# Performance work log

Hardware: AMD Instinct MI355X
Metric: run time of the kernel (lower is better)

Reference implementation:

```python
import jax, jax.numpy as jnp
import numpy as np

N, E, ND, ED, H, OUT, L, VC = 10000, 160000, 8, 4, 128, 256, 6, 6
HEADS, C = 4, 128  # GATConv: out_channels=128 per head, concat=False -> mean over heads


def _ln(x, g, b, eps=1e-5):
    m = x.mean(-1, keepdims=True)
    v = ((x - m) ** 2).mean(-1, keepdims=True)
    return (x - m) * jax.lax.rsqrt(v + eps) * g + b


def _gat_layer(h, src, dst, e_attr, lw, a_src, a_dst, lew, a_edge, bias):
    # h: [N,H]; e_attr: [Etot,H]; PyG GATConv(heads=4, concat=False, edge_dim=H)
    xh = (h @ lw).reshape(N, HEADS, C)                 # [N,4,128]
    eh = (e_attr @ lew).reshape(-1, HEADS, C)          # [Etot,4,128]
    al_s = jnp.einsum('nhc,hc->nh', xh, a_src)
    al_d = jnp.einsum('nhc,hc->nh', xh, a_dst)
    al_e = jnp.einsum('ehc,hc->eh', eh, a_edge)
    alpha = jax.nn.leaky_relu(al_s[src] + al_d[dst] + al_e, 0.2)  # [Etot,4]
    amax = jax.ops.segment_max(alpha, dst, num_segments=N)
    ex = jnp.exp(alpha - amax[dst])
    den = jax.ops.segment_sum(ex, dst, num_segments=N)
    w = ex / (den[dst] + 1e-16)
    out = jax.ops.segment_sum(xh[src] * w[..., None], dst, num_segments=N)  # [N,4,128]
    return out.mean(axis=1) + bias


def setup_inputs() -> dict:
    key = jax.random.key(0)
    ks = jax.random.split(key, 32)
    s = 0.05
    d = {
        'x': jax.random.normal(ks[0], (N, ND), jnp.float32),
        'edge_index': jax.random.randint(ks[1], (2, E), 0, N),
        'edge_attr': jax.random.uniform(ks[2], (E, ED), jnp.float32),
        'vnf_context': jax.random.normal(ks[3], (1, VC), jnp.float32),
        # node embedding
        'node_w': jax.random.normal(ks[4], (ND, H)) * s, 'node_b': jnp.zeros((H,)),
        # EdgeAttentionLayer
        'ea_proj_w': jax.random.normal(ks[5], (ED, H)) * s, 'ea_proj_b': jnp.zeros((H,)),
        'vnf_w': jax.random.normal(ks[6], (VC, H)) * s, 'vnf_b': jnp.zeros((H,)),
        'att1_w': jax.random.normal(ks[7], (2 * H, H)) * s, 'att1_b': jnp.zeros((H,)),
        'att2_w': jax.random.normal(ks[8], (H, H // 2)) * s, 'att2_b': jnp.zeros((H // 2,)),
        'att3_w': jax.random.normal(ks[9], (H // 2, 1)) * s, 'att3_b': jnp.zeros((1,)),
        # per-layer GATConv params (stacked over L layers)
        'gat_lin_w': jax.random.normal(ks[10], (L, H, HEADS * C)) * s,
        'gat_att_src': jax.random.normal(ks[11], (L, HEADS, C)) * s,
        'gat_att_dst': jax.random.normal(ks[12], (L, HEADS, C)) * s,
        'gat_lin_edge_w': jax.random.normal(ks[13], (L, H, HEADS * C)) * s,
        'gat_att_edge': jax.random.normal(ks[14], (L, HEADS, C)) * s,
        'gat_bias': jnp.zeros((L, C)),
        'ln_scale': jnp.ones((L, H)), 'ln_bias': jnp.zeros((L, H)),
        # output projection
        'out_w': jax.random.normal(ks[15], (H, OUT)) * s, 'out_b': jnp.zeros((OUT,)),
    }
    return d


def reference(x, edge_index, edge_attr, vnf_context, node_w, node_b, ea_proj_w, ea_proj_b,
              vnf_w, vnf_b, att1_w, att1_b, att2_w, att2_b, att3_w, att3_b,
              gat_lin_w, gat_att_src, gat_att_dst, gat_lin_edge_w, gat_att_edge, gat_bias,
              ln_scale, ln_bias, out_w, out_b):
    src, dst = edge_index[0], edge_index[1]
    h = x @ node_w + node_b                                   # [N,128]
    # EdgeAttentionLayer (eval mode, no network_state)
    ef = edge_attr @ ea_proj_w + ea_proj_b                    # [E,128]
    vnf = vnf_context @ vnf_w + vnf_b                         # [1,128]
    comb = jnp.concatenate([ef, jnp.broadcast_to(vnf, (E, H))], axis=-1)
    a = jax.nn.relu(comb @ att1_w + att1_b)
    a = jax.nn.relu(a @ att2_w + att2_b)
    e_gate = jax.nn.sigmoid(a @ att3_w + att3_b)              # [E,1]
    w_edge = ef * e_gate                                      # [E,128]
    # GATConv default add_self_loops=True, fill_value='mean'
    loop = jnp.arange(N)
    src2 = jnp.concatenate([src, loop])
    dst2 = jnp.concatenate([dst, loop])
    e2 = jnp.concatenate([w_edge, jnp.broadcast_to(w_edge.mean(0, keepdims=True), (N, H))], axis=0)
    for l in range(L):
        hc = _gat_layer(h, src2, dst2, e2, gat_lin_w[l], gat_att_src[l], gat_att_dst[l],
                        gat_lin_edge_w[l], gat_att_edge[l], gat_bias[l])
        h = _ln(h + jax.nn.relu(hc), ln_scale[l], ln_bias[l])
    return h @ out_w + out_b                                  # [N,256]
```

## Files before the change

### kernel.cpp

```cpp
#include <hip/hip_runtime.h>
#include <hip/hip_bf16.h>
#include <math.h>

#define Nn 10000
#define Ee 160000
#define ET 170000
#define LL 6

typedef short v8s __attribute__((ext_vector_type(8)));
typedef float v4f __attribute__((ext_vector_type(4)));
typedef float v2f __attribute__((ext_vector_type(2)));

__device__ __forceinline__ unsigned short f2bf(float v) {
    unsigned int b = __float_as_uint(v);
    b += 0x7fffu + ((b >> 16) & 1u);
    return (unsigned short)(b >> 16);
}
__device__ __forceinline__ float bflo(unsigned int u) { return __uint_as_float(u << 16); }
__device__ __forceinline__ float bfhi(unsigned int u) { return __uint_as_float(u & 0xffff0000u); }

__global__ void k_node_embed(const float* __restrict__ x, const float* __restrict__ nw,
                             const float* __restrict__ nb, float* __restrict__ h,
                             unsigned short* __restrict__ hb) {
    int idx = blockIdx.x * 256 + threadIdx.x;
    if (idx >= Nn * 128) return;
    int n = idx >> 7, c = idx & 127;
    const float* xr = x + (size_t)n * 8;
    float acc = nb[c];
#pragma unroll
    for (int k = 0; k < 8; k++) acc += xr[k] * nw[k * 128 + c];
    h[idx] = acc;
    hb[idx] = f2bf(acc);
}

__global__ void k_small(const float* __restrict__ vnfc, const float* __restrict__ vw,
                        const float* __restrict__ vb, const float* __restrict__ eab,
                        const float* __restrict__ a1w, const float* __restrict__ a1b,
                        const float* __restrict__ eaw, float* __restrict__ E1) {
    __shared__ float vr[128];
    __shared__ float sM1[512];
    __shared__ float sd1[128];
    int t = threadIdx.x;
    if (t < 128) {
        float a = vb[t];
#pragma unroll
        for (int k = 0; k < 6; k++) a += vnfc[k] * vw[k * 128 + t];
        vr[t] = a;
    }
    __syncthreads();
    if (t < 128) {
        float a = a1b[t];
        for (int k = 0; k < 128; k++) a += eab[k] * a1w[k * 128 + t];
        for (int k = 0; k < 128; k++) a += vr[k] * a1w[(128 + k) * 128 + t];
        sd1[t] = a;
    }
    {
        int r = t >> 7, j = t & 127;
        float a = 0.f;
        for (int k = 0; k < 128; k++) a += eaw[r * 128 + k] * a1w[k * 128 + j];
        sM1[r * 128 + j] = a;
    }
    __syncthreads();
    if (t < 128) {
        E1[t * 8 + 0] = sM1[t];
        E1[t * 8 + 1] = sM1[128 + t];
        E1[t * 8 + 2] = sM1[256 + t];
        E1[t * 8 + 3] = sM1[384 + t];
        E1[t * 8 + 4] = sd1[t];
        E1[t * 8 + 5] = 0.f; E1[t * 8 + 6] = 0.f; E1[t * 8 + 7] = 0.f;
    }
}

__global__ void k_bmat(const float* __restrict__ glw, const float* __restrict__ gas,
                       const float* __restrict__ gad, const float* __restrict__ glew,
                       const float* __restrict__ gae, float* __restrict__ Bs,
                       float* __restrict__ Bd, float* __restrict__ Be) {
    int idx = blockIdx.x * 256 + threadIdx.x;
    if (idx >= LL * 128 * 4) return;
    int hh = idx & 3, k = (idx >> 2) & 127, l = idx >> 9;
    const float* lwp = glw  + (size_t)l * 65536 + k * 512 + hh * 128;
    const float* lep = glew + (size_t)l * 65536 + k * 512 + hh * 128;
    const float* sp = gas + l * 512 + hh * 128;
    const float* dp = gad + l * 512 + hh * 128;
    const float* ep = gae + l * 512 + hh * 128;
    float s1 = 0, s2 = 0, s3 = 0;
    for (int c = 0; c < 128; c++) {
        float lv = lwp[c];
        s1 += lv * sp[c];
        s2 += lv * dp[c];
        s3 += lep[c] * ep[c];
    }
    Bs[idx] = s1; Bd[idx] = s2; Be[idx] = s3;
}

__global__ void k_wsum(const float* __restrict__ glw, unsigned short* __restrict__ WsumT) {
    int idx = blockIdx.x * 256 + threadIdx.x;
    if (idx >= LL * 128 * 512) return;
    int kk = idx & 511;
    int c = (idx >> 9) & 127;
    int l = idx >> 16;
    float v = 0.25f * glw[(size_t)l * 65536 + (size_t)(kk & 127) * 512 + (kk >> 7) * 128 + c];
    WsumT[(size_t)l * 65536 + (size_t)c * 512 + kk] = f2bf(v);
}

__global__ void k_w2b(const float* __restrict__ a2w, unsigned short* __restrict__ w2bf) {
    int idx = blockIdx.x * 256 + threadIdx.x;
    if (idx >= 8192) return;
    int j = idx & 7, lane = (idx >> 3) & 63, nt = (idx >> 9) & 3, ks = idx >> 11;
    int k = ks * 32 + ((lane >> 4) << 3) + j;
    int n = nt * 16 + (lane & 15);
    w2bf[idx] = f2bf(a2w[k * 64 + n]);
}

__global__ void k_pb(const float* __restrict__ eaw, const float* __restrict__ eab,
                     const float* __restrict__ Be, float* __restrict__ PB,
                     float* __restrict__ cB) {
    int t = threadIdx.x;
    if (t >= 24) return;
    int l = t >> 2, hh = t & 3;
    const float* bp = Be + l * 512 + hh;
    float s0 = 0, s1 = 0, s2 = 0, s3 = 0, sc = 0;
    for (int k = 0; k < 128; k++) {
        float bv = bp[k * 4];
        s0 += eaw[0 * 128 + k] * bv;
        s1 += eaw[1 * 128 + k] * bv;
        s2 += eaw[2 * 128 + k] * bv;
        s3 += eaw[3 * 128 + k] * bv;
        sc += eab[k] * bv;
    }
    PB[0 * 24 + t] = s0; PB[1 * 24 + t] = s1;
    PB[2 * 24 + t] = s2; PB[3 * 24 + t] = s3;
    cB[t] = sc;
}

__global__ __launch_bounds__(256, 2) void k_edge(
    const float* __restrict__ ea, const float* __restrict__ E1,
    const unsigned short* __restrict__ w2bf,
    const float* __restrict__ a2b, const float* __restrict__ a3w,
    const float* __restrict__ a3b,
    const float* __restrict__ PB, const float* __restrict__ cB,
    float* __restrict__ aleT, float* __restrict__ gsum) {
    __shared__ float4 sM[128];
    __shared__ float sD[128];
    __shared__ float4 sevs[256];
    __shared__ float gsh[256];
    __shared__ float sgsum[5];
    int t = threadIdx.x;
    int lane = t & 63;
    int wid = t >> 6;
    int c = lane & 15, q = lane >> 4;
    int eb0 = blockIdx.x * 256;

    sevs[t] = *(const float4*)(ea + (size_t)(eb0 + t) * 4);
    if (t < 128) {
        int slot = t ^ ((t >> 3) & 3);
        sM[slot] = *(const float4*)(E1 + t * 8);
        sD[t] = E1[t * 8 + 4];
    }
    if (t < 5) sgsum[t] = 0.f;
    __syncthreads();

    float4 ev4[4];
#pragma unroll
    for (int mt = 0; mt < 4; mt++) ev4[mt] = sevs[(wid * 4 + mt) * 16 + c];

    v8s av[4][4];
#pragma unroll
    for (int ks = 0; ks < 4; ks++) {
        float4 mr[8]; float dr[8];
#pragma unroll
        for (int j = 0; j < 8; j++) {
            int k = ks * 32 + q * 8 + j;
            mr[j] = sM[k ^ q];
            dr[j] = sD[k];
        }
#pragma unroll
        for (int mt = 0; mt < 4; mt++) {
            float4 ev = ev4[mt];
            v8s a;
#pragma unroll
            for (int j = 0; j < 8; j++) {
                float xv = fmaxf(dr[j] + ev.x * mr[j].x + ev.y * mr[j].y
                                       + ev.z * mr[j].z + ev.w * mr[j].w, 0.f);
                a[j] = (short)f2bf(xv);
            }
            av[mt][ks] = a;
        }
    }

    v4f acc[4][4];
#pragma unroll
    for (int nt = 0; nt < 4; nt++) {
        float bb = a2b[nt * 16 + c];
#pragma unroll
        for (int mt = 0; mt < 4; mt++) acc[mt][nt] = (v4f){bb, bb, bb, bb};
    }
#pragma unroll
    for (int nt = 0; nt < 4; nt++) {
#pragma unroll
        for (int ks = 0; ks < 4; ks++) {
            v8s b = *(const v8s*)(w2bf + ((size_t)(ks * 4 + nt) * 64 + lane) * 8);
#pragma unroll
            for (int mt = 0; mt < 4; mt++)
                acc[mt][nt] = __builtin_amdgcn_mfma_f32_16x16x32_bf16(av[mt][ks], b, acc[mt][nt], 0, 0, 0);
        }
    }

    float a3r[4];
#pragma unroll
    for (int nt = 0; nt < 4; nt++) a3r[nt] = a3w[nt * 16 + c];
    float a3b0 = a3b[0];
#pragma unroll
    for (int mt = 0; mt < 4; mt++) {
#pragma unroll
        for (int r = 0; r < 4; r++) {
            float s = 0.f;
#pragma unroll
            for (int nt = 0; nt < 4; nt++) s += fmaxf(acc[mt][nt][r], 0.f) * a3r[nt];
            s += __shfl_xor(s, 1); s += __shfl_xor(s, 2);
            s += __shfl_xor(s, 4); s += __shfl_xor(s, 8);
            if (c == 0) gsh[(wid * 4 + mt) * 16 + q * 4 + r] = 1.f / (1.f + __expf(-(s + a3b0)));
        }
    }
    __syncthreads();

    float g = gsh[t];
    float4 evv = sevs[t];
    float v0 = g, v1 = g * evv.x, v2 = g * evv.y, v3 = g * evv.z, v4 = g * evv.w;
#pragma unroll
    for (int d = 32; d > 0; d >>= 1) {
        v0 += __shfl_down(v0, d); v1 += __shfl_down(v1, d); v2 += __shfl_down(v2, d);
        v3 += __shfl_down(v3, d); v4 += __shfl_down(v4, d);
    }
    if (lane == 0) {
        atomicAdd(&sgsum[0], v0); atomicAdd(&sgsum[1], v1); atomicAdd(&sgsum[2], v2);
        atomicAdd(&sgsum[3], v3); atomicAdd(&sgsum[4], v4);
    }
    __syncthreads();
    if (t < 5) atomicAdd(&gsum[t], sgsum[t]);
#pragma unroll
    for (int i4 = 0; i4 < 6; i4++) {
        float4 cc = *(const float4*)(cB + i4 * 4);
        float4 p0 = *(const float4*)(PB + 0 * 24 + i4 * 4);
        float4 p1 = *(const float4*)(PB + 1 * 24 + i4 * 4);
        float4 p2 = *(const float4*)(PB + 2 * 24 + i4 * 4);
        float4 p3 = *(const float4*)(PB + 3 * 24 + i4 * 4);
        float4 o;
        o.x = g * (cc.x + evv.x * p0.x + evv.y * p1.x + evv.z * p2.x + evv.w * p3.x);
        o.y = g * (cc.y + evv.x * p0.y + evv.y * p1.y + evv.z * p2.y + evv.w * p3.y);
        o.z = g * (cc.z + evv.x * p0.z + evv.y * p1.z + evv.z * p2.z + evv.w * p3.z);
        o.w = g * (cc.w + evv.x * p0.w + evv.y * p1.w + evv.z * p2.w + evv.w * p3.w);
        *(float4*)(aleT + (size_t)i4 * Ee * 4 + (size_t)(eb0 + t) * 4) = o;
    }
}

__global__ void k_lale(const float* __restrict__ gsum, const float* __restrict__ PB,
                       const float* __restrict__ cB, float* __restrict__ lale) {
    int t = threadIdx.x;
    if (t >= 24) return;
    float s = gsum[0] * cB[t] + gsum[1] * PB[t] + gsum[2] * PB[24 + t]
            + gsum[3] * PB[48 + t] + gsum[4] * PB[72 + t];
    lale[t] = s * (1.0f / Ee);
}

__global__ void k_hist(const int* __restrict__ ei, int* __restrict__ hist) {
    int i = blockIdx.x * 256 + threadIdx.x;
    if (i >= ET) return;
    int d = (i < Ee) ? ei[Ee + i] : (i - Ee);
    atomicAdd(&hist[d], 1);
}

__global__ __launch_bounds__(1024) void k_scan(const int* __restrict__ hist,
                                               int* __restrict__ seg, int* __restrict__ pos) {
    __shared__ int wsums[16];
    __shared__ int carry_s;
    int t = threadIdx.x;
    int lane = t & 63, wid = t >> 6;
    if (t == 0) { carry_s = 0; seg[0] = 0; }
    __syncthreads();
    for (int base = 0; base < Nn; base += 1024) {
        int idx = base + t;
        int v = (idx < Nn) ? hist[idx] : 0;
        int sc = v;
#pragma unroll
        for (int d = 1; d < 64; d <<= 1) {
            int up = __shfl_up(sc, d);
            if (lane >= d) sc += up;
        }
        if (lane == 63) wsums[wid] = sc;
        __syncthreads();
        if (wid == 0) {
            int wv = (lane < 16) ? wsums[lane] : 0;
            int wsc = wv;
#pragma unroll
            for (int d = 1; d < 16; d <<= 1) {
                int up = __shfl_up(wsc, d);
                if (lane >= d) wsc += up;
            }
            if (lane < 16) wsums[lane] = wsc - wv;
        }
        __syncthreads();
        int carry = carry_s;
        int inc = sc + wsums[wid] + carry;
        if (idx < Nn) { seg[idx + 1] = inc; pos[idx] = inc - v; }
        __syncthreads();
        if (t == 1023) carry_s = inc;
        __syncthreads();
    }
}

__global__ void k_scatter(const int* __restrict__ ei, int* __restrict__ pos,
                          int2* __restrict__ pse) {
    int i = blockIdx.x * 256 + threadIdx.x;
    if (i >= ET) return;
    int s, d;
    if (i < Ee) { s = ei[i]; d = ei[Ee + i]; } else { s = d = i - Ee; }
    int idx = atomicAdd(&pos[d], 1);
    pse[idx] = make_int2(s, i);
}

__global__ void k_ab(const float* __restrict__ h, const float* __restrict__ Bs_l,
                     const float* __restrict__ Bd_l, float* __restrict__ als,
                     float* __restrict__ ald) {
    int idx = blockIdx.x * 256 + threadIdx.x;
    if (idx >= Nn * 8) return;
    int n = idx >> 3, slot = idx & 7;
    const float* B = (slot < 4) ? Bs_l : Bd_l;
    int hh = slot & 3;
    const float4* hr = (const float4*)(h + (size_t)n * 128);
    float s = 0.f;
#pragma unroll 8
    for (int kb = 0; kb < 32; kb++) {
        float4 hv = hr[kb];
        s += hv.x * B[(4 * kb + 0) * 4 + hh] + hv.y * B[(4 * kb + 1) * 4 + hh]
           + hv.z * B[(4 * kb + 2) * 4 + hh] + hv.w * B[(4 * kb + 3) * 4 + hh];
    }
    if (slot < 4) als[n * 4 + hh] = s;
    else          ald[n * 4 + hh] = s;
}

__global__ __launch_bounds__(256) void k_agg3(
    const int2* __restrict__ pse, const int* __restrict__ seg,
    const float* __restrict__ als, const float* __restrict__ ald,
    const float* __restrict__ aleT_l, const float* __restrict__ lale_l,
    const unsigned short* __restrict__ hb, unsigned short* __restrict__ aggb) {
    __shared__ float part[2][512];
    __shared__ float pden[2][4];
    int t = threadIdx.x;
    int lane = t & 63;
    int wv = (t >> 6) & 1;
    int w = t >> 7;
    int n = blockIdx.x * 2 + w;
    int start = seg[n], end = seg[n + 1];
    int deg = end - start;
    int half = (deg + 1) >> 1;
    int s0 = start + wv * half;
    int e0 = wv ? end : start + half;
    int hp = lane >> 4;
    int cch = (lane & 15) * 8;
    float aldh = ald[n * 4 + hp];
    float llh = lale_l[hp];
    float den = 0.f;
    float4 acc0 = make_float4(0.f, 0.f, 0.f, 0.f);
    float4 acc1 = make_float4(0.f, 0.f, 0.f, 0.f);
    int i = s0;
    for (; i + 2 <= e0; i += 2) {
        int2 sa = pse[i], sb = pse[i + 1];
        float ala = sa.y < Ee ? aleT_l[(size_t)sa.y * 4 + hp] : llh;
        float alb = sb.y < Ee ? aleT_l[(size_t)sb.y * 4 + hp] : llh;
        float ava = als[sa.x * 4 + hp] + aldh + ala;
        float avb = als[sb.x * 4 + hp] + aldh + alb;
        ava = ava > 0.f ? ava : 0.2f * ava;
        avb = avb > 0.f ? avb : 0.2f * avb;
        float ea = __expf(fminf(ava, 60.f));
        float eb = __expf(fminf(avb, 60.f));
        den += ea + eb;
        uint4 ua = *(const uint4*)(hb + (size_t)sa.x * 128 + cch);
        uint4 ub = *(const uint4*)(hb + (size_t)sb.x * 128 + cch);
        acc0.x += ea * bflo(ua.x) + eb * bflo(ub.x);
        acc0.y += ea * bfhi(ua.x) + eb * bfhi(ub.x);
        acc0.z += ea * bflo(ua.y) + eb * bflo(ub.y);
        acc0.w += ea * bfhi(ua.y) + eb * bfhi(ub.y);
        acc1.x += ea * bflo(ua.z) + eb * bflo(ub.z);
        acc1.y += ea * bfhi(ua.z) + eb * bfhi(ub.z);
        acc1.z += ea * bflo(ua.w) + eb * bflo(ub.w);
        acc1.w += ea * bfhi(ua.w) + eb * bfhi(ub.w);
    }
    if (i < e0) {
        int2 sa = pse[i];
        float ala = sa.y < Ee ? aleT_l[(size_t)sa.y * 4 + hp] : llh;
        float ava = als[sa.x * 4 + hp] + aldh + ala;
        ava = ava > 0.f ? ava : 0.2f * ava;
        float ea = __expf(fminf(ava, 60.f));
        den += ea;
        uint4 ua = *(const uint4*)(hb + (size_t)sa.x * 128 + cch);
        acc0.x += ea * bflo(ua.x); acc0.y += ea * bfhi(ua.x);
        acc0.z += ea * bflo(ua.y); acc0.w += ea * bfhi(ua.y);
        acc1.x += ea * bflo(ua.z); acc1.y += ea * bfhi(ua.z);
        acc1.z += ea * bflo(ua.w); acc1.w += ea * bfhi(ua.w);
    }
    if (wv == 1) {
        *(float4*)&part[w][lane * 8] = acc0;
        *(float4*)&part[w][lane * 8 + 4] = acc1;
        if ((lane & 15) == 0) pden[w][hp] = den;
    }
    __syncthreads();
    if (wv == 0) {
        float4 p0 = *(const float4*)&part[w][lane * 8];
        float4 p1 = *(const float4*)&part[w][lane * 8 + 4];
        float inv = 1.f / (den + pden[w][hp] + 1e-16f);
        acc0.x = (acc0.x + p0.x) * inv; acc0.y = (acc0.y + p0.y) * inv;
        acc0.z = (acc0.z + p0.z) * inv; acc0.w = (acc0.w + p0.w) * inv;
        acc1.x = (acc1.x + p1.x) * inv; acc1.y = (acc1.y + p1.y) * inv;
        acc1.z = (acc1.z + p1.z) * inv; acc1.w = (acc1.w + p1.w) * inv;
        ushort4 q0, q1;
        q0.x = f2bf(acc0.x); q0.y = f2bf(acc0.y); q0.z = f2bf(acc0.z); q0.w = f2bf(acc0.w);
        q1.x = f2bf(acc1.x); q1.y = f2bf(acc1.y); q1.z = f2bf(acc1.z); q1.w = f2bf(acc1.w);
        *(ushort4*)(aggb + (size_t)n * 512 + lane * 8) = q0;
        *(ushort4*)(aggb + (size_t)n * 512 + lane * 8 + 4) = q1;
    }
}

__global__ __launch_bounds__(256) void k_post(
    const unsigned short* __restrict__ aggb, const unsigned short* __restrict__ WsumT_l,
    const float* __restrict__ gbias, const float* __restrict__ lnsc,
    const float* __restrict__ lnbi, float* __restrict__ h,
    unsigned short* __restrict__ hb, const float* __restrict__ Bs_n,
    const float* __restrict__ Bd_n, float* __restrict__ als, float* __restrict__ ald) {
    int t = threadIdx.x;
    int lane = t & 63, w = t >> 6;
    int n0 = (blockIdx.x * 4 + w) * 16;
    if (n0 >= Nn) return;
    int m = lane & 15, q = lane >> 4;
    v4f acc[8];
#pragma unroll
    for (int nt = 0; nt < 8; nt++) acc[nt] = (v4f){0.f, 0.f, 0.f, 0.f};
    const unsigned short* arow = aggb + (size_t)(n0 + m) * 512 + q * 8;
#pragma unroll 4
    for (int ks = 0; ks < 16; ks++) {
        v8s fa = *(const v8s*)(arow + ks * 32);
#pragma unroll
        for (int nt = 0; nt < 8; nt++) {
            int col = nt * 16 + m;
            v8s fb = *(const v8s*)(WsumT_l + (size_t)col * 512 + ks * 32 + q * 8);
            acc[nt] = __builtin_amdgcn_mfma_f32_16x16x32_bf16(fa, fb, acc[nt], 0, 0, 0);
        }
    }
    float v[8][4];
    float s1[4] = {0.f, 0.f, 0.f, 0.f}, s2[4] = {0.f, 0.f, 0.f, 0.f};
#pragma unroll
    for (int nt = 0; nt < 8; nt++) {
        int col = nt * 16 + m;
        float b = gbias[col];
#pragma unroll
        for (int r = 0; r < 4; r++) {
            int row = n0 + q * 4 + r;
            float val = h[(size_t)row * 128 + col] + fmaxf(acc[nt][r] + b, 0.f);
            v[nt][r] = val;
            s1[r] += val; s2[r] += val * val;
        }
    }
#pragma unroll
    for (int d = 1; d <= 8; d <<= 1) {
#pragma unroll
        for (int r = 0; r < 4; r++) {
            s1[r] += __shfl_xor(s1[r], d);
            s2[r] += __shfl_xor(s2[r], d);
        }
    }
    float o8[8][4];
#pragma unroll
    for (int r = 0; r < 4; r++) {
        float mean = s1[r] * (1.f / 128.f);
        float var = s2[r] * (1.f / 128.f) - mean * mean;
        float rinv = rsqrtf(var + 1e-5f);
        int row = n0 + q * 4 + r;
#pragma unroll
        for (int nt = 0; nt < 8; nt++) {
            int col = nt * 16 + m;
            float o = (v[nt][r] - mean) * rinv * lnsc[col] + lnbi[col];
            o8[nt][r] = o;
            h[(size_t)row * 128 + col] = o;
            hb[(size_t)row * 128 + col] = f2bf(o);
        }
    }
    float sal[4][4], sad[4][4];
#pragma unroll
    for (int r = 0; r < 4; r++) {
#pragma unroll
        for (int hh = 0; hh < 4; hh++) { sal[r][hh] = 0.f; sad[r][hh] = 0.f; }
    }
#pragma unroll
    for (int nt = 0; nt < 8; nt++) {
        int col = nt * 16 + m;
        float4 bs = *(const float4*)(Bs_n + col * 4);
        float4 bd = *(const float4*)(Bd_n + col * 4);
#pragma unroll
// ... 20 lines not shown
        int hh = m & 3;
#pragma unroll
        for (int r = 0; r < 4; r++) {
            int row = n0 + q * 4 + r;
            float va = (hh == 0) ? sal[r][0] : (hh == 1) ? sal[r][1] : (hh == 2) ? sal[r][2] : sal[r][3];
            float vd = (hh == 0) ? sad[r][0] : (hh == 1) ? sad[r][1] : (hh == 2) ? sad[r][2] : sad[r][3];
            if (m < 4) als[row * 4 + hh] = va;
            else       ald[row * 4 + hh] = vd;
        }
    }
}

__global__ __launch_bounds__(256) void k_out(
    const float* __restrict__ h, const float* __restrict__ ow,
    const float* __restrict__ ob, float* __restrict__ out) {
    __shared__ float4 hs4[8][32];
    int t = threadIdx.x;
    int n0 = blockIdx.x * 8;
    if (t < 256) {
        int i = t >> 5, kb = t & 31;
        hs4[i][kb] = *(const float4*)(h + (size_t)(n0 + i) * 128 + 4 * kb);
    }
    __syncthreads();
    float acc[8] = {0, 0, 0, 0, 0, 0, 0, 0};
    for (int kb = 0; kb < 32; kb++) {
        float w0 = ow[(4 * kb + 0) * 256 + t];
        float w1 = ow[(4 * kb + 1) * 256 + t];
        float w2 = ow[(4 * kb + 2) * 256 + t];
        float w3 = ow[(4 * kb + 3) * 256 + t];
#pragma unroll
        for (int i = 0; i < 8; i++) {
            float4 hv = hs4[i][kb];
            acc[i] += hv.x * w0 + hv.y * w1 + hv.z * w2 + hv.w * w3;
        }
    }
    float b = ob[t];
#pragma unroll
    for (int i = 0; i < 8; i++) out[(size_t)(n0 + i) * 256 + t] = acc[i] + b;
}

extern "C" void kernel_launch(void* const* d_in, const int* in_sizes, int n_in,
                              void* d_out, int out_size, void* d_ws, size_t ws_size,
                              hipStream_t stream) {
    const float* x    = (const float*)d_in[0];
    const int*   ei   = (const int*)d_in[1];
    const float* ea   = (const float*)d_in[2];
    const float* vnfc = (const float*)d_in[3];
    const float* nw   = (const float*)d_in[4];
    const float* nb   = (const float*)d_in[5];
    const float* eaw  = (const float*)d_in[6];
    const float* eab  = (const float*)d_in[7];
    const float* vw   = (const float*)d_in[8];
    const float* vb   = (const float*)d_in[9];
    const float* a1w  = (const float*)d_in[10];
    const float* a1b  = (const float*)d_in[11];
    const float* a2w  = (const float*)d_in[12];
    const float* a2b  = (const float*)d_in[13];
    const float* a3w  = (const float*)d_in[14];
    const float* a3b  = (const float*)d_in[15];
    const float* glw  = (const float*)d_in[16];
    const float* gas  = (const float*)d_in[17];
    const float* gad  = (const float*)d_in[18];
    const float* glew = (const float*)d_in[19];
    const float* gae  = (const float*)d_in[20];
    const float* gb   = (const float*)d_in[21];
    const float* lnsc = (const float*)d_in[22];
    const float* lnbi = (const float*)d_in[23];
    const float* ow   = (const float*)d_in[24];
    const float* ob   = (const float*)d_in[25];
    float* out = (float*)d_out;

    char* w = (char*)d_ws;
    size_t o = 0;
    auto allocf = [&](size_t cnt) { float* p = (float*)(w + o); o += ((cnt * 4 + 255) / 256) * 256; return p; };
    auto alloci = [&](size_t cnt) { int* p = (int*)(w + o); o += ((cnt * 4 + 255) / 256) * 256; return p; };
    auto allocu = [&](size_t cnt) { unsigned short* p = (unsigned short*)(w + o); o += ((cnt * 2 + 255) / 256) * 256; return p; };
    float* h      = allocf((size_t)Nn * 128);
    unsigned short* hb    = allocu((size_t)Nn * 128);
    unsigned short* aggb  = allocu((size_t)Nn * 512);
    unsigned short* WsumT = allocu((size_t)LL * 128 * 512);
    unsigned short* w2bf  = allocu(8192);
    float* als    = allocf((size_t)Nn * 4);
    float* ald    = allocf((size_t)Nn * 4);
    float* aleT   = allocf((size_t)LL * Ee * 4);
    float* Bs     = allocf(3072);
    float* Bd     = allocf(3072);
    float* Be     = allocf(3072);
    float* E1     = allocf(1024);
    float* PB     = allocf(96);
    float* cB     = allocf(24);
    float* gsum   = allocf(8);
    float* lale   = allocf(32);
    int* seg  = alloci(Nn + 1);
    int* hist = alloci(Nn);
    int* pos  = alloci(Nn);
    int2* pse = (int2*)alloci((size_t)ET * 2);

    hipMemsetAsync(hist, 0, Nn * sizeof(int), stream);
    hipMemsetAsync(gsum, 0, 8 * sizeof(float), stream);

    k_node_embed<<<(Nn * 128 + 255) / 256, 256, 0, stream>>>(x, nw, nb, h, hb);
    k_small<<<1, 512, 0, stream>>>(vnfc, vw, vb, eab, a1w, a1b, eaw, E1);
    k_bmat<<<(LL * 128 * 4 + 255) / 256, 256, 0, stream>>>(glw, gas, gad, glew, gae, Bs, Bd, Be);
    k_wsum<<<(LL * 128 * 512 + 255) / 256, 256, 0, stream>>>(glw, WsumT);
    k_w2b<<<32, 256, 0, stream>>>(a2w, w2bf);
    k_pb<<<1, 32, 0, stream>>>(eaw, eab, Be, PB, cB);
    k_edge<<<Ee / 256, 256, 0, stream>>>(ea, E1, w2bf, a2b, a3w, a3b, PB, cB, aleT, gsum);
    k_hist<<<(ET + 255) / 256, 256, 0, stream>>>(ei, hist);
    k_scan<<<1, 1024, 0, stream>>>(hist, seg, pos);
    k_scatter<<<(ET + 255) / 256, 256, 0, stream>>>(ei, pos, pse);
    k_lale<<<1, 32, 0, stream>>>(gsum, PB, cB, lale);
    k_ab<<<(Nn * 8 + 255) / 256, 256, 0, stream>>>(h, Bs, Bd, als, ald);
    for (int l = 0; l < LL; l++) {
        int ln = (l + 1) % LL;
        k_agg3<<<Nn / 2, 256, 0, stream>>>(pse, seg, als, ald, aleT + (size_t)l * Ee * 4,
                                           lale + l * 4, hb, aggb);
        k_post<<<(625 + 3) / 4, 256, 0, stream>>>(aggb, WsumT + (size_t)l * 65536,
                                                  gb + l * 128, lnsc + l * 128, lnbi + l * 128,
                                                  h, hb, Bs + ln * 512, Bd + ln * 512, als, ald);
    }
    k_out<<<Nn / 8, 256, 0, stream>>>(h, ow, ob, out);
}
```

Baseline: 515.2 us.

## Store edge attention terms in CSR order and merge setup kernels

k_edge now writes each edge's attention logits straight into its dst-sorted CSR slot, using an inverse permutation built by k_scatter. The mean-filled self-loop logits are written into their slots by a new k_abfill kernel, which also computes als/ald. k_agg3 therefore reads contiguous per-slot logits and a plain src index array, with no indirect gather through the original edge id and no self-loop branch. Separately, many small setup kernels (embedding, histogram, B matrices, Wsum, w2b, E1, PB) are merged into two launches to cut launch overhead. In exchange, k_edge does scattered writes and the scatter pass must finish before it.

```diff
diff --git a/kernel.cpp b/kernel.cpp
--- a/kernel.cpp
+++ b/kernel.cpp
@@ -9,7 +9,6 @@
 
 typedef short v8s __attribute__((ext_vector_type(8)));
 typedef float v4f __attribute__((ext_vector_type(4)));
-typedef float v2f __attribute__((ext_vector_type(2)));
 
 __device__ __forceinline__ unsigned short f2bf(float v) {
     unsigned int b = __float_as_uint(v);
@@ -19,255 +18,133 @@
 __device__ __forceinline__ float bflo(unsigned int u) { return __uint_as_float(u << 16); }
 __device__ __forceinline__ float bfhi(unsigned int u) { return __uint_as_float(u & 0xffff0000u); }
 
-__global__ void k_node_embed(const float* __restrict__ x, const float* __restrict__ nw,
-                             const float* __restrict__ nb, float* __restrict__ h,
-                             unsigned short* __restrict__ hb) {
-    int idx = blockIdx.x * 256 + threadIdx.x;
-    if (idx >= Nn * 128) return;
-    int n = idx >> 7, c = idx & 127;
-    const float* xr = x + (size_t)n * 8;
-    float acc = nb[c];
-#pragma unroll
-    for (int k = 0; k < 8; k++) acc += xr[k] * nw[k * 128 + c];
-    h[idx] = acc;
-    hb[idx] = f2bf(acc);
-}
-
-__global__ void k_small(const float* __restrict__ vnfc, const float* __restrict__ vw,
-                        const float* __restrict__ vb, const float* __restrict__ eab,
-                        const float* __restrict__ a1w, const float* __restrict__ a1b,
-                        const float* __restrict__ eaw, float* __restrict__ E1) {
+__global__ __launch_bounds__(256) void k_first(
+    const float* __restrict__ x, const float* __restrict__ nw,
+    const float* __restrict__ nb, float* __restrict__ h, unsigned short* __restrict__ hb,
+    const int* __restrict__ ei, int* __restrict__ hist,
+    const float* __restrict__ glw, const float* __restrict__ gas,
+    const float* __restrict__ gad, const float* __restrict__ glew,
+    const float* __restrict__ gae, float* __restrict__ Bs,
+    float* __restrict__ Bd, float* __restrict__ Be) {
+    int b = blockIdx.x, t = threadIdx.x;
+    if (b < 5000) {
+        int idx = b * 256 + t;
+        int n = idx >> 7, c = idx & 127;
+        const float* xr = x + (size_t)n * 8;
+        float acc = nb[c];
+#pragma unroll
+        for (int k = 0; k < 8; k++) acc += xr[k] * nw[k * 128 + c];
+        h[idx] = acc;
+        hb[idx] = f2bf(acc);
+        return;
+    }
+    if (b < 5665) {
+        int i = (b - 5000) * 256 + t;
+        if (i < ET) {
+            int d = (i < Ee) ? ei[Ee + i] : (i - Ee);
+            atomicAdd(&hist[d], 1);
+        }
+        return;
+    }
+    {
+        int idx = (b - 5665) * 256 + t;
+        if (idx >= LL * 128 * 4) return;
+        int hh = idx & 3, k = (idx >> 2) & 127, l = idx >> 9;
+        const float* lwp = glw  + (size_t)l * 65536 + k * 512 + hh * 128;
+        const float* lep = glew + (size_t)l * 65536 + k * 512 + hh * 128;
+        const float* sp = gas + l * 512 + hh * 128;
+        const float* dp = gad + l * 512 + hh * 128;
+        const float* ep = gae + l * 512 + hh * 128;
+        float s1 = 0, s2 = 0, s3 = 0;
+        for (int c = 0; c < 128; c++) {
+            float lv = lwp[c];
+            s1 += lv * sp[c];
+            s2 += lv * dp[c];
+            s3 += lep[c] * ep[c];
+        }
+        Bs[idx] = s1; Bd[idx] = s2; Be[idx] = s3;
+    }
+}
+
+__global__ __launch_bounds__(256) void k_setup(
+    const float* __restrict__ glw, unsigned short* __restrict__ WsumT,
+    const float* __restrict__ a2w, unsigned short* __restrict__ w2bf,
+    const float* __restrict__ vnfc, const float* __restrict__ vw,
+    const float* __restrict__ vb, const float* __restrict__ eab,
+    const float* __restrict__ a1w, const float* __restrict__ a1b,
+    const float* __restrict__ eaw, float* __restrict__ E1,
+    const float* __restrict__ Be, float* __restrict__ PB, float* __restrict__ cB) {
     __shared__ float vr[128];
     __shared__ float sM1[512];
     __shared__ float sd1[128];
-    int t = threadIdx.x;
-    if (t < 128) {
-        float a = vb[t];
-#pragma unroll
-        for (int k = 0; k < 6; k++) a += vnfc[k] * vw[k * 128 + t];
-        vr[t] = a;
-    }
-    __syncthreads();
-    if (t < 128) {
-        float a = a1b[t];
-        for (int k = 0; k < 128; k++) a += eab[k] * a1w[k * 128 + t];
-        for (int k = 0; k < 128; k++) a += vr[k] * a1w[(128 + k) * 128 + t];
-        sd1[t] = a;
+    int b = blockIdx.x, t = threadIdx.x;
+    if (b < 1536) {
+        int idx = b * 256 + t;
+        int kk = idx & 511;
+        int c = (idx >> 9) & 127;
+        int l = idx >> 16;
+        float v = 0.25f * glw[(size_t)l * 65536 + (size_t)(kk & 127) * 512 + (kk >> 7) * 128 + c];
+        WsumT[(size_t)l * 65536 + (size_t)c * 512 + kk] = f2bf(v);
+        return;
+    }
+    if (b < 1568) {
+        int idx = (b - 1536) * 256 + t;
+        int j = idx & 7, lane = (idx >> 3) & 63, nt = (idx >> 9) & 3, ks = idx >> 11;
+        int k = ks * 32 + ((lane >> 4) << 3) + j;
+        int n = nt * 16 + (lane & 15);
+        w2bf[idx] = f2bf(a2w[k * 64 + n]);
+        return;
+    }
+    if (b == 1568) {
+        if (t < 128) {
+            float a = vb[t];
+#pragma unroll
+            for (int k = 0; k < 6; k++) a += vnfc[k] * vw[k * 128 + t];
+            vr[t] = a;
+        }
+        __syncthreads();
+        if (t < 128) {
+            float a = a1b[t];
+            for (int k = 0; k < 128; k++) a += eab[k] * a1w[k * 128 + t];
+            for (int k = 0; k < 128; k++) a += vr[k] * a1w[(128 + k) * 128 + t];
+            sd1[t] = a;
+        }
+#pragma unroll
+        for (int rr = 0; rr < 2; rr++) {
+            int id = rr * 256 + t;
+            int r = id >> 7, j = id & 127;
+            float a = 0.f;
+            for (int k = 0; k < 128; k++) a += eaw[r * 128 + k] * a1w[k * 128 + j];
+            sM1[id] = a;
+        }
+        __syncthreads();
+        if (t < 128) {
+            E1[t * 8 + 0] = sM1[t];
+            E1[t * 8 + 1] = sM1[128 + t];
+            E1[t * 8 + 2] = sM1[256 + t];
+            E1[t * 8 + 3] = sM1[384 + t];
+            E1[t * 8 + 4] = sd1[t];
+            E1[t * 8 + 5] = 0.f; E1[t * 8 + 6] = 0.f; E1[t * 8 + 7] = 0.f;
+        }
+        return;
     }
     {
-        int r = t >> 7, j = t & 127;
-        float a = 0.f;
-        for (int k = 0; k < 128; k++) a += eaw[r * 128 + k] * a1w[k * 128 + j];
-        sM1[r * 128 + j] = a;
-    }
-    __syncthreads();
-    if (t < 128) {
-        E1[t * 8 + 0] = sM1[t];
-        E1[t * 8 + 1] = sM1[128 + t];
-        E1[t * 8 + 2] = sM1[256 + t];
-        E1[t * 8 + 3] = sM1[384 + t];
-        E1[t * 8 + 4] = sd1[t];
-        E1[t * 8 + 5] = 0.f; E1[t * 8 + 6] = 0.f; E1[t * 8 + 7] = 0.f;
-    }
-}
-
-__global__ void k_bmat(const float* __restrict__ glw, const float* __restrict__ gas,
-                       const float* __restrict__ gad, const float* __restrict__ glew,
-                       const float* __restrict__ gae, float* __restrict__ Bs,
-                       float* __restrict__ Bd, float* __restrict__ Be) {
-    int idx = blockIdx.x * 256 + threadIdx.x;
-    if (idx >= LL * 128 * 4) return;
-    int hh = idx & 3, k = (idx >> 2) & 127, l = idx >> 9;
-    const float* lwp = glw  + (size_t)l * 65536 + k * 512 + hh * 128;
-    const float* lep = glew + (size_t)l * 65536 + k * 512 + hh * 128;
-    const float* sp = gas + l * 512 + hh * 128;
-    const float* dp = gad + l * 512 + hh * 128;
-    const float* ep = gae + l * 512 + hh * 128;
-    float s1 = 0, s2 = 0, s3 = 0;
-    for (int c = 0; c < 128; c++) {
-        float lv = lwp[c];
-        s1 += lv * sp[c];
-        s2 += lv * dp[c];
-        s3 += lep[c] * ep[c];
-    }
-    Bs[idx] = s1; Bd[idx] = s2; Be[idx] = s3;
-}
-
-__global__ void k_wsum(const float* __restrict__ glw, unsigned short* __restrict__ WsumT) {
-    int idx = blockIdx.x * 256 + threadIdx.x;
-    if (idx >= LL * 128 * 512) return;
-    int kk = idx & 511;
-    int c = (idx >> 9) & 127;
-    int l = idx >> 16;
-    float v = 0.25f * glw[(size_t)l * 65536 + (size_t)(kk & 127) * 512 + (kk >> 7) * 128 + c];
-    WsumT[(size_t)l * 65536 + (size_t)c * 512 + kk] = f2bf(v);
-}
-
-__global__ void k_w2b(const float* __restrict__ a2w, unsigned short* __restrict__ w2bf) {
-    int idx = blockIdx.x * 256 + threadIdx.x;
-    if (idx >= 8192) return;
-    int j = idx & 7, lane = (idx >> 3) & 63, nt = (idx >> 9) & 3, ks = idx >> 11;
-    int k = ks * 32 + ((lane >> 4) << 3) + j;
-    int n = nt * 16 + (lane & 15);
-    w2bf[idx] = f2bf(a2w[k * 64 + n]);
-}
-
-__global__ void k_pb(const float* __restrict__ eaw, const float* __restrict__ eab,
-                     const float* __restrict__ Be, float* __restrict__ PB,
-                     float* __restrict__ cB) {
-    int t = threadIdx.x;
-    if (t >= 24) return;
-    int l = t >> 2, hh = t & 3;
-    const float* bp = Be + l * 512 + hh;
-    float s0 = 0, s1 = 0, s2 = 0, s3 = 0, sc = 0;
-    for (int k = 0; k < 128; k++) {
-        float bv = bp[k * 4];
-        s0 += eaw[0 * 128 + k] * bv;
-        s1 += eaw[1 * 128 + k] * bv;
-        s2 += eaw[2 * 128 + k] * bv;
-        s3 += eaw[3 * 128 + k] * bv;
-        sc += eab[k] * bv;
-    }
-    PB[0 * 24 + t] = s0; PB[1 * 24 + t] = s1;
-    PB[2 * 24 + t] = s2; PB[3 * 24 + t] = s3;
-    cB[t] = sc;
-}
-
-__global__ __launch_bounds__(256, 2) void k_edge(
-    const float* __restrict__ ea, const float* __restrict__ E1,
-    const unsigned short* __restrict__ w2bf,
-    const float* __restrict__ a2b, const float* __restrict__ a3w,
-    const float* __restrict__ a3b,
-    const float* __restrict__ PB, const float* __restrict__ cB,
-    float* __restrict__ aleT, float* __restrict__ gsum) {
-    __shared__ float4 sM[128];
-    __shared__ float sD[128];
-    __shared__ float4 sevs[256];
-    __shared__ float gsh[256];
-    __shared__ float sgsum[5];
-    int t = threadIdx.x;
-    int lane = t & 63;
-    int wid = t >> 6;
-    int c = lane & 15, q = lane >> 4;
-    int eb0 = blockIdx.x * 256;
-
-    sevs[t] = *(const float4*)(ea + (size_t)(eb0 + t) * 4);
-    if (t < 128) {
-        int slot = t ^ ((t >> 3) & 3);
-        sM[slot] = *(const float4*)(E1 + t * 8);
-        sD[t] = E1[t * 8 + 4];
-    }
-    if (t < 5) sgsum[t] = 0.f;
-    __syncthreads();
-
-    float4 ev4[4];
-#pragma unroll
-    for (int mt = 0; mt < 4; mt++) ev4[mt] = sevs[(wid * 4 + mt) * 16 + c];
-
-    v8s av[4][4];
-#pragma unroll
-    for (int ks = 0; ks < 4; ks++) {
-        float4 mr[8]; float dr[8];
-#pragma unroll
-        for (int j = 0; j < 8; j++) {
-            int k = ks * 32 + q * 8 + j;
-            mr[j] = sM[k ^ q];
-            dr[j] = sD[k];
-        }
-#pragma unroll
-        for (int mt = 0; mt < 4; mt++) {
-            float4 ev = ev4[mt];
-            v8s a;
-#pragma unroll
-            for (int j = 0; j < 8; j++) {
-                float xv = fmaxf(dr[j] + ev.x * mr[j].x + ev.y * mr[j].y
-                                       + ev.z * mr[j].z + ev.w * mr[j].w, 0.f);
-                a[j] = (short)f2bf(xv);
-            }
-            av[mt][ks] = a;
-        }
-    }
-
-    v4f acc[4][4];
-#pragma unroll
-    for (int nt = 0; nt < 4; nt++) {
-        float bb = a2b[nt * 16 + c];
-#pragma unroll
-        for (int mt = 0; mt < 4; mt++) acc[mt][nt] = (v4f){bb, bb, bb, bb};
-    }
-#pragma unroll
-    for (int nt = 0; nt < 4; nt++) {
-#pragma unroll
-        for (int ks = 0; ks < 4; ks++) {
-            v8s b = *(const v8s*)(w2bf + ((size_t)(ks * 4 + nt) * 64 + lane) * 8);
-#pragma unroll
-            for (int mt = 0; mt < 4; mt++)
-                acc[mt][nt] = __builtin_amdgcn_mfma_f32_16x16x32_bf16(av[mt][ks], b, acc[mt][nt], 0, 0, 0);
-        }
-    }
-
-    float a3r[4];
-#pragma unroll
-    for (int nt = 0; nt < 4; nt++) a3r[nt] = a3w[nt * 16 + c];
-    float a3b0 = a3b[0];
-#pragma unroll
-    for (int mt = 0; mt < 4; mt++) {
-#pragma unroll
-        for (int r = 0; r < 4; r++) {
-            float s = 0.f;
-#pragma unroll
-            for (int nt = 0; nt < 4; nt++) s += fmaxf(acc[mt][nt][r], 0.f) * a3r[nt];
-            s += __shfl_xor(s, 1); s += __shfl_xor(s, 2);
-            s += __shfl_xor(s, 4); s += __shfl_xor(s, 8);
-            if (c == 0) gsh[(wid * 4 + mt) * 16 + q * 4 + r] = 1.f / (1.f + __expf(-(s + a3b0)));
-        }
-    }
-    __syncthreads();
-
-    float g = gsh[t];
-    float4 evv = sevs[t];
-    float v0 = g, v1 = g * evv.x, v2 = g * evv.y, v3 = g * evv.z, v4 = g * evv.w;
-#pragma unroll
-    for (int d = 32; d > 0; d >>= 1) {
-        v0 += __shfl_down(v0, d); v1 += __shfl_down(v1, d); v2 += __shfl_down(v2, d);
-        v3 += __shfl_down(v3, d); v4 += __shfl_down(v4, d);
-    }
-    if (lane == 0) {
-        atomicAdd(&sgsum[0], v0); atomicAdd(&sgsum[1], v1); atomicAdd(&sgsum[2], v2);
-        atomicAdd(&sgsum[3], v3); atomicAdd(&sgsum[4], v4);
-    }
-    __syncthreads();
-    if (t < 5) atomicAdd(&gsum[t], sgsum[t]);
-#pragma unroll
-    for (int i4 = 0; i4 < 6; i4++) {
-        float4 cc = *(const float4*)(cB + i4 * 4);
-        float4 p0 = *(const float4*)(PB + 0 * 24 + i4 * 4);
-        float4 p1 = *(const float4*)(PB + 1 * 24 + i4 * 4);
-        float4 p2 = *(const float4*)(PB + 2 * 24 + i4 * 4);
-        float4 p3 = *(const float4*)(PB + 3 * 24 + i4 * 4);
-        float4 o;
-        o.x = g * (cc.x + evv.x * p0.x + evv.y * p1.x + evv.z * p2.x + evv.w * p3.x);
-        o.y = g * (cc.y + evv.x * p0.y + evv.y * p1.y + evv.z * p2.y + evv.w * p3.y);
-        o.z = g * (cc.z + evv.x * p0.z + evv.y * p1.z + evv.z * p2.z + evv.w * p3.z);
-        o.w = g * (cc.w + evv.x * p0.w + evv.y * p1.w + evv.z * p2.w + evv.w * p3.w);
-        *(float4*)(aleT + (size_t)i4 * Ee * 4 + (size_t)(eb0 + t) * 4) = o;
-    }
-}
-
-__global__ void k_lale(const float* __restrict__ gsum, const float* __restrict__ PB,
-                       const float* __restrict__ cB, float* __restrict__ lale) {
-    int t = threadIdx.x;
-    if (t >= 24) return;
-    float s = gsum[0] * cB[t] + gsum[1] * PB[t] + gsum[2] * PB[24 + t]
-            + gsum[3] * PB[48 + t] + gsum[4] * PB[72 + t];
-    lale[t] = s * (1.0f / Ee);
-}
-
-__global__ void k_hist(const int* __restrict__ ei, int* __restrict__ hist) {
-    int i = blockIdx.x * 256 + threadIdx.x;
-    if (i >= ET) return;
-    int d = (i < Ee) ? ei[Ee + i] : (i - Ee);
-    atomicAdd(&hist[d], 1);
+        if (t >= 24) return;
+        int l = t >> 2, hh = t & 3;
+        const float* bp = Be + l * 512 + hh;
+        float s0 = 0, s1 = 0, s2 = 0, s3 = 0, sc = 0;
+        for (int k = 0; k < 128; k++) {
+            float bv = bp[k * 4];
+            s0 += eaw[0 * 128 + k] * bv;
+            s1 += eaw[1 * 128 + k] * bv;
+            s2 += eaw[2 * 128 + k] * bv;
+            s3 += eaw[3 * 128 + k] * bv;
+            sc += eab[k] * bv;
+        }
+        PB[0 * 24 + t] = s0; PB[1 * 24 + t] = s1;
+        PB[2 * 24 + t] = s2; PB[3 * 24 + t] = s3;
+        cB[t] = sc;
+    }
 }
 
 __global__ __launch_bounds__(1024) void k_scan(const int* __restrict__ hist,
@@ -310,39 +187,191 @@
 }
 
 __global__ void k_scatter(const int* __restrict__ ei, int* __restrict__ pos,
-                          int2* __restrict__ pse) {
+                          int* __restrict__ srcv, int* __restrict__ inv,
+                          int* __restrict__ loopslot) {
     int i = blockIdx.x * 256 + threadIdx.x;
     if (i >= ET) return;
     int s, d;
     if (i < Ee) { s = ei[i]; d = ei[Ee + i]; } else { s = d = i - Ee; }
     int idx = atomicAdd(&pos[d], 1);
-    pse[idx] = make_int2(s, i);
-}
-
-__global__ void k_ab(const float* __restrict__ h, const float* __restrict__ Bs_l,
-                     const float* __restrict__ Bd_l, float* __restrict__ als,
-                     float* __restrict__ ald) {
-    int idx = blockIdx.x * 256 + threadIdx.x;
-    if (idx >= Nn * 8) return;
-    int n = idx >> 3, slot = idx & 7;
-    const float* B = (slot < 4) ? Bs_l : Bd_l;
-    int hh = slot & 3;
-    const float4* hr = (const float4*)(h + (size_t)n * 128);
-    float s = 0.f;
+    srcv[idx] = s;
+    if (i < Ee) inv[i] = idx;
+    else        loopslot[i - Ee] = idx;
+}
+
+__global__ __launch_bounds__(256, 2) void k_edge(
+    const float* __restrict__ ea, const float* __restrict__ E1,
+    const unsigned short* __restrict__ w2bf,
+    const float* __restrict__ a2b, const float* __restrict__ a3w,
+    const float* __restrict__ a3b,
+    const float* __restrict__ PB, const float* __restrict__ cB,
+    const int* __restrict__ inv,
+    float* __restrict__ aleT, float* __restrict__ gsum) {
+    __shared__ float4 sM[128];
+    __shared__ float sD[128];
+    __shared__ float4 sevs[256];
+    __shared__ float gsh[256];
+    __shared__ float sgsum[5];
+    int t = threadIdx.x;
+    int lane = t & 63;
+    int wid = t >> 6;
+    int c = lane & 15, q = lane >> 4;
+    int eb0 = blockIdx.x * 256;
+
+    sevs[t] = *(const float4*)(ea + (size_t)(eb0 + t) * 4);
+    if (t < 128) {
+        int slot = t ^ ((t >> 3) & 3);
+        sM[slot] = *(const float4*)(E1 + t * 8);
+        sD[t] = E1[t * 8 + 4];
+    }
+    if (t < 5) sgsum[t] = 0.f;
+    __syncthreads();
+
+    float4 ev4[4];
+#pragma unroll
+    for (int mt = 0; mt < 4; mt++) ev4[mt] = sevs[(wid * 4 + mt) * 16 + c];
+
+    v8s av[4][4];
+#pragma unroll
+    for (int ks = 0; ks < 4; ks++) {
+        float4 mr[8]; float dr[8];
+#pragma unroll
+        for (int j = 0; j < 8; j++) {
+            int k = ks * 32 + q * 8 + j;
+            mr[j] = sM[k ^ q];
+            dr[j] = sD[k];
+        }
+#pragma unroll
+        for (int mt = 0; mt < 4; mt++) {
+            float4 ev = ev4[mt];
+            v8s a;
+#pragma unroll
+            for (int j = 0; j < 8; j++) {
+                float xv = fmaxf(dr[j] + ev.x * mr[j].x + ev.y * mr[j].y
+                                       + ev.z * mr[j].z + ev.w * mr[j].w, 0.f);
+                a[j] = (short)f2bf(xv);
+            }
+            av[mt][ks] = a;
+        }
+    }
+
+    v4f acc[4][4];
+#pragma unroll
+    for (int nt = 0; nt < 4; nt++) {
+        float bb = a2b[nt * 16 + c];
+#pragma unroll
+        for (int mt = 0; mt < 4; mt++) acc[mt][nt] = (v4f){bb, bb, bb, bb};
+    }
+#pragma unroll
+    for (int nt = 0; nt < 4; nt++) {
+#pragma unroll
+        for (int ks = 0; ks < 4; ks++) {
+            v8s bfr = *(const v8s*)(w2bf + ((size_t)(ks * 4 + nt) * 64 + lane) * 8);
+#pragma unroll
+            for (int mt = 0; mt < 4; mt++)
+                acc[mt][nt] = __builtin_amdgcn_mfma_f32_16x16x32_bf16(av[mt][ks], bfr, acc[mt][nt], 0, 0, 0);
+        }
+    }
+
+    float a3r[4];
+#pragma unroll
+    for (int nt = 0; nt < 4; nt++) a3r[nt] = a3w[nt * 16 + c];
+    float a3b0 = a3b[0];
+#pragma unroll
+    for (int mt = 0; mt < 4; mt++) {
+#pragma unroll
+        for (int r = 0; r < 4; r++) {
+            float s = 0.f;
+#pragma unroll
+            for (int nt = 0; nt < 4; nt++) s += fmaxf(acc[mt][nt][r], 0.f) * a3r[nt];
+            s += __shfl_xor(s, 1); s += __shfl_xor(s, 2);
+            s += __shfl_xor(s, 4); s += __shfl_xor(s, 8);
+            if (c == 0) gsh[(wid * 4 + mt) * 16 + q * 4 + r] = 1.f / (1.f + __expf(-(s + a3b0)));
+        }
+    }
+    __syncthreads();
+
+    float g = gsh[t];
+    float4 evv = sevs[t];
+    float v0 = g, v1 = g * evv.x, v2 = g * evv.y, v3 = g * evv.z, v4 = g * evv.w;
+#pragma unroll
+    for (int d = 32; d > 0; d >>= 1) {
+        v0 += __shfl_down(v0, d); v1 += __shfl_down(v1, d); v2 += __shfl_down(v2, d);
+        v3 += __shfl_down(v3, d); v4 += __shfl_down(v4, d);
+    }
+    if (lane == 0) {
+        atomicAdd(&sgsum[0], v0); atomicAdd(&sgsum[1], v1); atomicAdd(&sgsum[2], v2);
+        atomicAdd(&sgsum[3], v3); atomicAdd(&sgsum[4], v4);
+    }
+    __syncthreads();
+    if (t < 5) atomicAdd(&gsum[t], sgsum[t]);
+    int slot = inv[eb0 + t];
+#pragma unroll
+    for (int i4 = 0; i4 < 6; i4++) {
+        float4 cc = *(const float4*)(cB + i4 * 4);
+        float4 p0 = *(const float4*)(PB + 0 * 24 + i4 * 4);
+        float4 p1 = *(const float4*)(PB + 1 * 24 + i4 * 4);
+        float4 p2 = *(const float4*)(PB + 2 * 24 + i4 * 4);
+        float4 p3 = *(const float4*)(PB + 3 * 24 + i4 * 4);
+        float4 o;
+        o.x = g * (cc.x + evv.x * p0.x + evv.y * p1.x + evv.z * p2.x + evv.w * p3.x);
+        o.y = g * (cc.y + evv.x * p0.y + evv.y * p1.y + evv.z * p2.y + evv.w * p3.y);
+        o.z = g * (cc.z + evv.x * p0.z + evv.y * p1.z + evv.z * p2.z + evv.w * p3.z);
+        o.w = g * (cc.w + evv.x * p0.w + evv.y * p1.w + evv.z * p2.w + evv.w * p3.w);
+        *(float4*)(aleT + (size_t)i4 * ET * 4 + (size_t)slot * 4) = o;
+    }
+}
+
+__global__ __launch_bounds__(256) void k_abfill(
+    const float* __restrict__ h, const float* __restrict__ Bs_l,
+    const float* __restrict__ Bd_l, float* __restrict__ als, float* __restrict__ ald,
+    const int* __restrict__ loopslot, const float* __restrict__ gsum,
+    const float* __restrict__ PB, const float* __restrict__ cB,
+    float* __restrict__ aleT) {
+    int b = blockIdx.x, t = threadIdx.x;
+    if (b < 313) {
+        int idx = b * 256 + t;
+        if (idx >= Nn * 8) return;
+        int n = idx >> 3, slot = idx & 7;
+        const float* B = (slot < 4) ? Bs_l : Bd_l;
+        int hh = slot & 3;
+        const float4* hr = (const float4*)(h + (size_t)n * 128);
+        float s = 0.f;
 #pragma unroll 8
-    for (int kb = 0; kb < 32; kb++) {
-        float4 hv = hr[kb];
-        s += hv.x * B[(4 * kb + 0) * 4 + hh] + hv.y * B[(4 * kb + 1) * 4 + hh]
-           + hv.z * B[(4 * kb + 2) * 4 + hh] + hv.w * B[(4 * kb + 3) * 4 + hh];
-    }
-    if (slot < 4) als[n * 4 + hh] = s;
-    else          ald[n * 4 + hh] = s;
+        for (int kb = 0; kb < 32; kb++) {
+            float4 hv = hr[kb];
+            s += hv.x * B[(4 * kb + 0) * 4 + hh] + hv.y * B[(4 * kb + 1) * 4 + hh]
+               + hv.z * B[(4 * kb + 2) * 4 + hh] + hv.w * B[(4 * kb + 3) * 4 + hh];
+        }
+        if (slot < 4) als[n * 4 + hh] = s;
+        else          ald[n * 4 + hh] = s;
+        return;
+    }
+    {
+        int idx = (b - 313) * 256 + t;
+        if (idx >= LL * Nn) return;
+        int l = idx / Nn;
+        int j = idx - l * Nn;
+        int slot = loopslot[j];
+        float g0 = gsum[0], g1 = gsum[1], g2 = gsum[2], g3 = gsum[3], g4 = gsum[4];
+        float4 cc = *(const float4*)(cB + l * 4);
+        float4 p0 = *(const float4*)(PB + 0 * 24 + l * 4);
+        float4 p1 = *(const float4*)(PB + 1 * 24 + l * 4);
+        float4 p2 = *(const float4*)(PB + 2 * 24 + l * 4);
+        float4 p3 = *(const float4*)(PB + 3 * 24 + l * 4);
+        float4 o;
+        o.x = (g0 * cc.x + g1 * p0.x + g2 * p1.x + g3 * p2.x + g4 * p3.x) * (1.0f / Ee);
+        o.y = (g0 * cc.y + g1 * p0.y + g2 * p1.y + g3 * p2.y + g4 * p3.y) * (1.0f / Ee);
+        o.z = (g0 * cc.z + g1 * p0.z + g2 * p1.z + g3 * p2.z + g4 * p3.z) * (1.0f / Ee);
+        o.w = (g0 * cc.w + g1 * p0.w + g2 * p1.w + g3 * p2.w + g4 * p3.w) * (1.0f / Ee);
+        *(float4*)(aleT + (size_t)l * ET * 4 + (size_t)slot * 4) = o;
+    }
 }
 
 __global__ __launch_bounds__(256) void k_agg3(
-    const int2* __restrict__ pse, const int* __restrict__ seg,
+    const int* __restrict__ srcv, const int* __restrict__ seg,
     const float* __restrict__ als, const float* __restrict__ ald,
-    const float* __restrict__ aleT_l, const float* __restrict__ lale_l,
+    const float* __restrict__ aleS_l,
     const unsigned short* __restrict__ hb, unsigned short* __restrict__ aggb) {
     __shared__ float part[2][512];
     __shared__ float pden[2][4];
@@ -359,24 +388,23 @@
     int hp = lane >> 4;
     int cch = (lane & 15) * 8;
     float aldh = ald[n * 4 + hp];
-    float llh = lale_l[hp];
     float den = 0.f;
     float4 acc0 = make_float4(0.f, 0.f, 0.f, 0.f);
     float4 acc1 = make_float4(0.f, 0.f, 0.f, 0.f);
     int i = s0;
     for (; i + 2 <= e0; i += 2) {
-        int2 sa = pse[i], sb = pse[i + 1];
-        float ala = sa.y < Ee ? aleT_l[(size_t)sa.y * 4 + hp] : llh;
-        float alb = sb.y < Ee ? aleT_l[(size_t)sb.y * 4 + hp] : llh;
-        float ava = als[sa.x * 4 + hp] + aldh + ala;
-        float avb = als[sb.x * 4 + hp] + aldh + alb;
+        int sa = srcv[i], sb = srcv[i + 1];
+        float ala = aleS_l[(size_t)i * 4 + hp];
+        float alb = aleS_l[(size_t)(i + 1) * 4 + hp];
+        float ava = als[sa * 4 + hp] + aldh + ala;
+        float avb = als[sb * 4 + hp] + aldh + alb;
         ava = ava > 0.f ? ava : 0.2f * ava;
         avb = avb > 0.f ? avb : 0.2f * avb;
         float ea = __expf(fminf(ava, 60.f));
         float eb = __expf(fminf(avb, 60.f));
         den += ea + eb;
-        uint4 ua = *(const uint4*)(hb + (size_t)sa.x * 128 + cch);
-        uint4 ub = *(const uint4*)(hb + (size_t)sb.x * 128 + cch);
+        uint4 ua = *(const uint4*)(hb + (size_t)sa * 128 + cch);
+        uint4 ub = *(const uint4*)(hb + (size_t)sb * 128 + cch);
         acc0.x += ea * bflo(ua.x) + eb * bflo(ub.x);
         acc0.y += ea * bfhi(ua.x) + eb * bfhi(ub.x);
         acc0.z += ea * bflo(ua.y) + eb * bflo(ub.y);
@@ -387,13 +415,13 @@
         acc1.w += ea * bfhi(ua.w) + eb * bfhi(ub.w);
     }
     if (i < e0) {
-        int2 sa = pse[i];
-        float ala = sa.y < Ee ? aleT_l[(size_t)sa.y * 4 + hp] : llh;
-        float ava = als[sa.x * 4 + hp] + aldh + ala;
+        int sa = srcv[i];
+        float ala = aleS_l[(size_t)i * 4 + hp];
+        float ava = als[sa * 4 + hp] + aldh + ala;
         ava = ava > 0.f ? ava : 0.2f * ava;
         float ea = __expf(fminf(ava, 60.f));
         den += ea;
-        uint4 ua = *(const uint4*)(hb + (size_t)sa.x * 128 + cch);
+        uint4 ua = *(const uint4*)(hb + (size_t)sa * 128 + cch);
         acc0.x += ea * bflo(ua.x); acc0.y += ea * bfhi(ua.x);
         acc0.z += ea * bflo(ua.y); acc0.w += ea * bfhi(ua.y);
         acc1.x += ea * bflo(ua.z); acc1.y += ea * bfhi(ua.z);
@@ -408,11 +436,11 @@
     if (wv == 0) {
         float4 p0 = *(const float4*)&part[w][lane * 8];
         float4 p1 = *(const float4*)&part[w][lane * 8 + 4];
-        float inv = 1.f / (den + pden[w][hp] + 1e-16f);
-        acc0.x = (acc0.x + p0.x) * inv; acc0.y = (acc0.y + p0.y) * inv;
-        acc0.z = (acc0.z + p0.z) * inv; acc0.w = (acc0.w + p0.w) * inv;
-        acc1.x = (acc1.x + p1.x) * inv; acc1.y = (acc1.y + p1.y) * inv;
-        acc1.z = (acc1.z + p1.z) * inv; acc1.w = (acc1.w + p1.w) * inv;
+        float inv2 = 1.f / (den + pden[w][hp] + 1e-16f);
+        acc0.x = (acc0.x + p0.x) * inv2; acc0.y = (acc0.y + p0.y) * inv2;
+        acc0.z = (acc0.z + p0.z) * inv2; acc0.w = (acc0.w + p0.w) * inv2;
+        acc1.x = (acc1.x + p1.x) * inv2; acc1.y = (acc1.y + p1.y) * inv2;
+        acc1.z = (acc1.z + p1.z) * inv2; acc1.w = (acc1.w + p1.w) * inv2;
         ushort4 q0, q1;
         q0.x = f2bf(acc0.x); q0.y = f2bf(acc0.y); q0.z = f2bf(acc0.z); q0.w = f2bf(acc0.w);
         q1.x = f2bf(acc1.x); q1.y = f2bf(acc1.y); q1.z = f2bf(acc1.z); q1.w = f2bf(acc1.w);
@@ -599,7 +627,7 @@
     unsigned short* w2bf  = allocu(8192);
     float* als    = allocf((size_t)Nn * 4);
     float* ald    = allocf((size_t)Nn * 4);
-    float* aleT   = allocf((size_t)LL * Ee * 4);
+    float* aleT   = allocf((size_t)LL * ET * 4);
     float* Bs     = allocf(3072);
     float* Bd     = allocf(3072);
     float* Be     = allocf(3072);
@@ -607,31 +635,28 @@
     float* PB     = allocf(96);
     float* cB     = allocf(24);
     float* gsum   = allocf(8);
-    float* lale   = allocf(32);
-    int* seg  = alloci(Nn + 1);
-    int* hist = alloci(Nn);
-    int* pos  = alloci(Nn);
-    int2* pse = (int2*)alloci((size_t)ET * 2);
+    int* seg      = alloci(Nn + 1);
+    int* hist     = alloci(Nn);
+    int* pos      = alloci(Nn);
+    int* srcv     = alloci(ET);
+    int* inv      = alloci(Ee);
+    int* loopslot = alloci(Nn);
 
     hipMemsetAsync(hist, 0, Nn * sizeof(int), stream);
     hipMemsetAsync(gsum, 0, 8 * sizeof(float), stream);
 
-    k_node_embed<<<(Nn * 128 + 255) / 256, 256, 0, stream>>>(x, nw, nb, h, hb);
-    k_small<<<1, 512, 0, stream>>>(vnfc, vw, vb, eab, a1w, a1b, eaw, E1);
-    k_bmat<<<(LL * 128 * 4 + 255) / 256, 256, 0, stream>>>(glw, gas, gad, glew, gae, Bs, Bd, Be);
-    k_wsum<<<(LL * 128 * 512 + 255) / 256, 256, 0, stream>>>(glw, WsumT);
-    k_w2b<<<32, 256, 0, stream>>>(a2w, w2bf);
-    k_pb<<<1, 32, 0, stream>>>(eaw, eab, Be, PB, cB);
-    k_edge<<<Ee / 256, 256, 0, stream>>>(ea, E1, w2bf, a2b, a3w, a3b, PB, cB, aleT, gsum);
-    k_hist<<<(ET + 255) / 256, 256, 0, stream>>>(ei, hist);
+    k_first<<<5677, 256, 0, stream>>>(x, nw, nb, h, hb, ei, hist,
+                                      glw, gas, gad, glew, gae, Bs, Bd, Be);
+    k_setup<<<1570, 256, 0, stream>>>(glw, WsumT, a2w, w2bf, vnfc, vw, vb, eab,
+                                      a1w, a1b, eaw, E1, Be, PB, cB);
     k_scan<<<1, 1024, 0, stream>>>(hist, seg, pos);
-    k_scatter<<<(ET + 255) / 256, 256, 0, stream>>>(ei, pos, pse);
-    k_lale<<<1, 32, 0, stream>>>(gsum, PB, cB, lale);
-    k_ab<<<(Nn * 8 + 255) / 256, 256, 0, stream>>>(h, Bs, Bd, als, ald);
+    k_scatter<<<(ET + 255) / 256, 256, 0, stream>>>(ei, pos, srcv, inv, loopslot);
+    k_edge<<<Ee / 256, 256, 0, stream>>>(ea, E1, w2bf, a2b, a3w, a3b, PB, cB, inv, aleT, gsum);
+    k_abfill<<<548, 256, 0, stream>>>(h, Bs, Bd, als, ald, loopslot, gsum, PB, cB, aleT);
     for (int l = 0; l < LL; l++) {
         int ln = (l + 1) % LL;
-        k_agg3<<<Nn / 2, 256, 0, stream>>>(pse, seg, als, ald, aleT + (size_t)l * Ee * 4,
-                                           lale + l * 4, hb, aggb);
+        k_agg3<<<Nn / 2, 256, 0, stream>>>(srcv, seg, als, ald,
+                                           aleT + (size_t)l * ET * 4, hb, aggb);
         k_post<<<(625 + 3) / 4, 256, 0, stream>>>(aggb, WsumT + (size_t)l * 65536,
                                                   gb + l * 128, lnsc + l * 128, lnbi + l * 128,
                                                   h, hb, Bs + ln * 512, Bd + ln * 512, als, ald);
```

Measured after the change: 497.8 us. 1.03x faster.
